# Optimization experiments

Measured on AMD Instinct MI355X. Metric: run time of the kernel, lower is better.

## Reference

```python
import jax, jax.numpy as jnp
import numpy as np

V, BS, E, H, L, FC = 50257, 1024, 768, 12, 6, 4
B, T = 4, 1024
HS = E // H
FF = FC * E
EPS = 1e-5


def setup_inputs() -> dict:
    key = jax.random.key(0)
    ks = jax.random.split(key, 24)
    s = 0.02
    inp = {
        'idx': jax.random.randint(ks[0], (B, T), 0, V),
        'targets': jax.random.randint(ks[1], (B, T), 0, V),
        'tok_emb': jax.random.normal(ks[2], (V, E), jnp.float32) * s,
        'pos_emb': jax.random.normal(ks[3], (BS, E), jnp.float32) * s,
        'Wq': jax.random.normal(ks[4], (L, H, E, HS), jnp.float32) * s,
        'Wk': jax.random.normal(ks[5], (L, H, E, HS), jnp.float32) * s,
        'Wv': jax.random.normal(ks[6], (L, H, E, HS), jnp.float32) * s,
        'Wo': jax.random.normal(ks[7], (L, E, E), jnp.float32) * s,
        'bo': jnp.zeros((L, E), jnp.float32),
        'ln1_s': jnp.ones((L, E), jnp.float32),
        'ln1_b': jnp.zeros((L, E), jnp.float32),
        'ln2_s': jnp.ones((L, E), jnp.float32),
        'ln2_b': jnp.zeros((L, E), jnp.float32),
        'W1': jax.random.normal(ks[8], (L, E, FF), jnp.float32) * s,
        'b1': jnp.zeros((L, FF), jnp.float32),
        'W2': jax.random.normal(ks[9], (L, FF, E), jnp.float32) * s,
        'b2': jnp.zeros((L, E), jnp.float32),
        'lnf_s': jnp.ones((E,), jnp.float32),
        'lnf_b': jnp.zeros((E,), jnp.float32),
        'Wlm': jax.random.normal(ks[10], (E, V), jnp.float32) * s,
        'blm': jnp.zeros((V,), jnp.float32),
    }
    return inp


def _ln(x, scale, bias):
    mu = x.mean(-1, keepdims=True)
    var = ((x - mu) ** 2).mean(-1, keepdims=True)
    return (x - mu) * jax.lax.rsqrt(var + EPS) * scale + bias


def _forward(idx, targets, tok_emb, pos_emb, Wq, Wk, Wv, Wo, bo,
             ln1_s, ln1_b, ln2_s, ln2_b, W1, b1, W2, b2,
             lnf_s, lnf_b, Wlm, blm):
    Bc, Tc = idx.shape
    x = tok_emb[idx] + pos_emb[:Tc]                      # [B,T,E]
    causal = jnp.tril(jnp.ones((Tc, Tc), bool))          # [T,T]

    def block(x, p):
        wq, wk, wv, wo_, bo_, l1s, l1b, l2s, l2b, w1, b1_, w2, b2_ = p
        h = _ln(x, l1s, l1b)
        q = jnp.einsum('bte,hed->bhtd', h, wq)
        k = jnp.einsum('bte,hed->bhtd', h, wk)
        v = jnp.einsum('bte,hed->bhtd', h, wv)
        scores = jnp.einsum('bhtd,bhsd->bhts', q, k) * (HS ** -0.5)
        scores = jnp.where(causal, scores, -jnp.inf)
        att = jax.nn.softmax(scores, axis=-1)            # [B,H,T,T]
        o = jnp.einsum('bhts,bhsd->bhtd', att, v)
        o = o.transpose(0, 2, 1, 3).reshape(Bc, Tc, E)   # concat heads
        x = x + jnp.einsum('bte,ef->btf', o, wo_) + bo_
        h2 = _ln(x, l2s, l2b)
        f = jax.nn.relu(jnp.einsum('bte,ef->btf', h2, w1) + b1_)
        x = x + jnp.einsum('btf,fe->bte', f, w2) + b2_
        return x, None

    layers = (Wq, Wk, Wv, Wo, bo, ln1_s, ln1_b, ln2_s, ln2_b, W1, b1, W2, b2)
    x, _ = jax.lax.scan(block, x, layers)
    x = _ln(x, lnf_s, lnf_b)
    logits = jnp.einsum('bte,ev->btv', x, Wlm) + blm     # [B,T,V]
    logp = jax.nn.log_softmax(logits, axis=-1)
    nll = -jnp.take_along_axis(logp, targets[..., None], axis=-1)[..., 0]
    loss = nll.mean()
    return logits, loss


def reference(idx, targets, tok_emb, pos_emb, Wq, Wk, Wv, Wo, bo,
              ln1_s, ln1_b, ln2_s, ln2_b, W1, b1, W2, b2,
              lnf_s, lnf_b, Wlm, blm):
    return _forward(idx, targets, tok_emb, pos_emb, Wq, Wk, Wv, Wo, bo,
                    ln1_s, ln1_b, ln2_s, ln2_b, W1, b1, W2, b2,
                    lnf_s, lnf_b, Wlm, blm)
```

## Files before the change

kernel.cpp:

```cpp
#include <hip/hip_runtime.h>
#include <hip/hip_bf16.h>
#include <cstdint>
#include <cstddef>

#define NB 4
#define NT 1024
#define NE 768
#define NH 12
#define NHS 64
#define NL 6
#define NFF 3072
#define NV 50257
#define NVP 50304
#define NTOK (NB*NT)
#define NCB_LM (NVP/128)
#define QKVS 2304

typedef __attribute__((ext_vector_type(8))) short short8;
typedef __attribute__((ext_vector_type(4))) float f32x4;
typedef __hip_bfloat16 bf16;

__global__ __launch_bounds__(256) void embed_kernel(
    const int* __restrict__ idx, const float* __restrict__ tok,
    const float* __restrict__ pos, float* __restrict__ x)
{
  int bt = blockIdx.x;
  int token = idx[bt];
  int t = bt & (NT - 1);
  const float* tr = tok + (size_t)token * NE;
  const float* pr = pos + (size_t)t * NE;
  float* xr = x + (size_t)bt * NE;
  for (int i = threadIdx.x; i < NE; i += 256)
    xr[i] = tr[i] + pr[i];
}

__global__ __launch_bounds__(256) void ln_kernel(
    const float* __restrict__ in, const float* __restrict__ sc,
    const float* __restrict__ bi, bf16* __restrict__ out)
{
  int row = blockIdx.x, tid = threadIdx.x;
  const float* xr = in + (size_t)row * NE;
  float v0 = xr[tid], v1 = xr[tid + 256], v2 = xr[tid + 512];
  float s = v0 + v1 + v2;
  float ss = v0 * v0 + v1 * v1 + v2 * v2;
  #pragma unroll
  for (int o = 32; o > 0; o >>= 1) {
    s  += __shfl_xor(s, o);
    ss += __shfl_xor(ss, o);
  }
  __shared__ float r1[4], r2[4];
  if ((tid & 63) == 0) { r1[tid >> 6] = s; r2[tid >> 6] = ss; }
  __syncthreads();
  float tot = r1[0] + r1[1] + r1[2] + r1[3];
  float tss = r2[0] + r2[1] + r2[2] + r2[3];
  float mu  = tot * (1.f / NE);
  float var = tss * (1.f / NE) - mu * mu;
  float rs  = rsqrtf(var + 1e-5f);
  bf16* orow = out + (size_t)row * NE;
  orow[tid]       = __float2bfloat16((v0 - mu) * rs * sc[tid]       + bi[tid]);
  orow[tid + 256] = __float2bfloat16((v1 - mu) * rs * sc[tid + 256] + bi[tid + 256]);
  orow[tid + 512] = __float2bfloat16((v2 - mu) * rs * sc[tid + 512] + bi[tid + 512]);
}

__global__ __launch_bounds__(256) void tconv_kernel(
    const float* __restrict__ src, bf16* __restrict__ dst,
    int R, int Cs, int Cd, int zdiv,
    size_t srcZstr, size_t dstLstr, size_t dstHstr)
{
  __shared__ float t[32][33];
  int z = blockIdx.z;
  int l = z / zdiv, h = z - l * zdiv;
  src += (size_t)z * srcZstr;
  dst += (size_t)l * dstLstr + (size_t)h * dstHstr;
  int c0 = blockIdx.x * 32, r0 = blockIdx.y * 32;
  int tx = threadIdx.x & 31, ty = threadIdx.x >> 5;
  #pragma unroll
  for (int i = 0; i < 32; i += 8) {
    int r = r0 + ty + i, c = c0 + tx;
    t[ty + i][tx] = (c < Cs) ? src[(size_t)r * Cs + c] : 0.f;
  }
  __syncthreads();
  #pragma unroll
  for (int i = 0; i < 32; i += 8) {
    int c = c0 + ty + i, r = r0 + tx;
    if (c < Cd) dst[(size_t)c * R + r] = __float2bfloat16(t[tx][ty + i]);
  }
}

template<int MREP, int DEPTH, bool SWZ>
__global__ __launch_bounds__(256) void pgemm(
    const bf16* __restrict__ A, const bf16* __restrict__ BT,
    float* __restrict__ Cf, bf16* __restrict__ Cbf,
    const float* __restrict__ bias, const float* __restrict__ Rres,
    float* __restrict__ ps,
    int M, int N, int K, int relu, int ncb)
{
  constexpr int BMT = MREP * 32;
  constexpr int AIT = (MREP * 128) / 256;
  constexpr int SWAIT = AIT + 2;
  __shared__ bf16 As[DEPTH][BMT][32];
  __shared__ bf16 Bs[DEPTH][128][32];
  __shared__ float ps2[BMT][2];
  int tid = threadIdx.x;
  int lane = tid & 63;
  int w = __builtin_amdgcn_readfirstlane(tid >> 6);
  int wr = w >> 1, wc = w & 1;
  int row0 = blockIdx.y * BMT;
  int col0 = blockIdx.x * 128;
  int l15 = lane & 15;
  int g8 = (lane >> 4) << 3;
  const int nk = K / 32;

  f32x4 acc[MREP][4] = {};

  auto STAGE = [&](int b, int t) {
    int k0 = t * 32;
    #pragma unroll
    for (int r = 0; r < AIT; ++r) {
      int c = r * 256 + tid;
      int trow = c >> 2;
      int sch = SWZ ? ((c & 3) ^ (trow & 3)) : (c & 3);
      const bf16* ga = A + (size_t)(row0 + trow) * K + k0 + (sch << 3);
      __builtin_amdgcn_global_load_lds(
          (const __attribute__((address_space(1))) void*)ga,
          (__attribute__((address_space(3))) void*)((char*)&As[b][0][0] + (unsigned)c * 16),
          16, 0, 0);
    }
    #pragma unroll
    for (int r = 0; r < 2; ++r) {
      int c = r * 256 + tid;
      int trow = c >> 2;
      int sch = SWZ ? ((c & 3) ^ (trow & 3)) : (c & 3);
      const bf16* gb = BT + (size_t)(col0 + trow) * K + k0 + (sch << 3);
      __builtin_amdgcn_global_load_lds(
          (const __attribute__((address_space(1))) void*)gb,
          (__attribute__((address_space(3))) void*)((char*)&Bs[b][0][0] + (unsigned)c * 16),
          16, 0, 0);
    }
  };

  STAGE(0, 0);
  if (DEPTH == 3 && nk > 1) STAGE(1, 1);

  for (int t = 0; t < nk; ++t) {
    if (DEPTH == 3 && t + 1 < nk) {
      if (SWAIT == 4) asm volatile("s_waitcnt vmcnt(4)" ::: "memory");
      else            asm volatile("s_waitcnt vmcnt(3)" ::: "memory");
    } else {
      asm volatile("s_waitcnt vmcnt(0)" ::: "memory");
    }
    __builtin_amdgcn_s_barrier();
    if (t + DEPTH - 1 < nk) STAGE((t + DEPTH - 1) % DEPTH, t + DEPTH - 1);

    int b = t % DEPTH;
    int sx = SWZ ? ((l15 & 3) << 3) : 0;
    short8 a[MREP], bb[4];
    #pragma unroll
    for (int m = 0; m < MREP; ++m)
      a[m] = *(const short8*)&As[b][wr * (MREP * 16) + m * 16 + l15][g8 ^ sx];
    #pragma unroll
    for (int n = 0; n < 4; ++n)
      bb[n] = *(const short8*)&Bs[b][wc * 64 + n * 16 + l15][g8 ^ sx];
    #pragma unroll
    for (int m = 0; m < MREP; ++m)
      #pragma unroll
      for (int n = 0; n < 4; ++n)
        acc[m][n] = __builtin_amdgcn_mfma_f32_16x16x32_bf16(a[m], bb[n], acc[m][n], 0, 0, 0);
  }

  int cr = lane >> 4;
  int cc = lane & 15;
  #pragma unroll
  for (int m = 0; m < MREP; ++m) {
    #pragma unroll
    for (int n = 0; n < 4; ++n) {
      int col = col0 + wc * 64 + n * 16 + cc;
      if (col >= N) continue;
      float bv = bias ? bias[col] : 0.f;
      #pragma unroll
      for (int e = 0; e < 4; ++e) {
        int row = row0 + wr * (MREP * 16) + m * 16 + cr * 4 + e;
        float v = acc[m][n][e] + bv;
        size_t off = (size_t)row * N + col;
        if (Rres) v += Rres[off];
        if (relu) v = fmaxf(v, 0.f);
        if (Cf)  Cf[off] = v;
        if (Cbf) Cbf[off] = __float2bfloat16(v);
      }
    }
  }

  if (ps) {
    #pragma unroll
    for (int m = 0; m < MREP; ++m) {
      #pragma unroll
      for (int e = 0; e < 4; ++e) {
        float ssum = 0.f;
        #pragma unroll
        for (int n = 0; n < 4; ++n) {
          int col = col0 + wc * 64 + n * 16 + cc;
          float val = (col < N) ? (acc[m][n][e] + (bias ? bias[col] : 0.f)) : -1e30f;
          ssum += __expf(val);
        }
        ssum += __shfl_xor(ssum, 1);
        ssum += __shfl_xor(ssum, 2);
        ssum += __shfl_xor(ssum, 4);
        ssum += __shfl_xor(ssum, 8);
        if (cc == 0) {
          int rl = wr * (MREP * 16) + m * 16 + cr * 4 + e;
          ps2[rl][wc] = ssum;
        }
      }
    }
    __syncthreads();
    for (int i = tid; i < BMT; i += 256) {
      size_t o = (size_t)(row0 + i) * ncb + blockIdx.x;
      ps[o] = ps2[i][0] + ps2[i][1];
    }
  }
}

static __device__ inline unsigned short bfbits(float x) {
  bf16 h = __float2bfloat16(x);
  return *reinterpret_cast<unsigned short*>(&h);
}

__global__ __launch_bounds__(256) void fattn_kernel(
    const bf16* __restrict__ QKV, bf16* __restrict__ O)
{
  __shared__ unsigned short Ks[64][72];
  __shared__ unsigned short Vt[64][72];
  __shared__ unsigned short Pl[4][16][72];
  int qt = blockIdx.x, h = blockIdx.y, b = blockIdx.z;
  int tid = threadIdx.x;
  int lane = tid & 63;
  int w = tid >> 6;
  int l15 = lane & 15, g = lane >> 4;
  int brow = b * NT;
  int qbase = qt * 64;
  int q_loc = w * 16 + l15;

  short8 bq[2];
  {
    const bf16* qp = QKV + (size_t)(brow + qbase + q_loc) * QKVS + h * 64 + g * 8;
    bq[0] = *(const short8*)qp;
    bq[1] = *(const short8*)(qp + 32);
  }

  float m_run = -1e30f, l_run = 0.f;
  f32x4 acc[4] = {};

  for (int kt = 0; kt <= qt; ++kt) {
    int s0 = kt * 64;
    #pragma unroll
    for (int i = 0; i < 2; ++i) {
      int c = tid + i * 256;
      int row = c >> 3, colg = (c & 7) * 8;
      const bf16* kp = QKV + (size_t)(brow + s0 + row) * QKVS + NE + h * 64 + colg;
      const bf16* vp = QKV + (size_t)(brow + s0 + row) * QKVS + 2 * NE + h * 64 + colg;
      short8 kv = *(const short8*)kp;
      short8 vv = *(const short8*)vp;
      *(short8*)&Ks[row][colg] = kv;
      #pragma unroll
      for (int j = 0; j < 8; ++j)
        Vt[colg + j][row] = (unsigned short)vv[j];
    }
    __syncthreads();

    f32x4 sf[4] = {};
    #pragma unroll
    for (int kk = 0; kk < 2; ++kk) {
      #pragma unroll
      for (int m = 0; m < 4; ++m) {
        short8 a = *(const short8*)&Ks[m * 16 + l15][kk * 32 + g * 8];
        sf[m] = __builtin_amdgcn_mfma_f32_16x16x32_bf16(a, bq[kk], sf[m], 0, 0, 0);
      }
    }

    float sv[4][4];
    float mx = -1e30f;
    bool diag = (kt == qt);
    #pragma unroll
    for (int m = 0; m < 4; ++m)
      #pragma unroll
      for (int e = 0; e < 4; ++e) {
        float v = sf[m][e] * 0.125f;
        if (diag) {
          int sl = m * 16 + g * 4 + e;
          if (sl > q_loc) v = -1e30f;
        }
        sv[m][e] = v;
        mx = fmaxf(mx, v);
      }
    mx = fmaxf(mx, __shfl_xor(mx, 16));
    mx = fmaxf(mx, __shfl_xor(mx, 32));
    float m_new = fmaxf(m_run, mx);
    float p[4][4];
    float rs = 0.f;
    #pragma unroll
    for (int m = 0; m < 4; ++m)
      #pragma unroll
      for (int e = 0; e < 4; ++e) {
        float pe = __expf(sv[m][e] - m_new);
        p[m][e] = pe;
        rs += pe;
      }
    rs += __shfl_xor(rs, 16);
    rs += __shfl_xor(rs, 32);
    float sc_old = __expf(m_run - m_new);
    l_run = l_run * sc_old + rs;
    m_run = m_new;
    #pragma unroll
    for (int dm = 0; dm < 4; ++dm)
      #pragma unroll
      for (int e = 0; e < 4; ++e)
        acc[dm][e] *= sc_old;

    #pragma unroll
    for (int m = 0; m < 4; ++m)
      #pragma unroll
      for (int ep = 0; ep < 2; ++ep) {
        unsigned u = (unsigned)bfbits(p[m][2 * ep]) |
                     ((unsigned)bfbits(p[m][2 * ep + 1]) << 16);
        *(unsigned*)&Pl[w][l15][m * 16 + g * 4 + ep * 2] = u;
      }

    #pragma unroll
    for (int ks = 0; ks < 2; ++ks) {
      short8 pb = *(const short8*)&Pl[w][l15][ks * 32 + g * 8];
      #pragma unroll
      for (int dm = 0; dm < 4; ++dm) {
        short8 av = *(const short8*)&Vt[dm * 16 + l15][ks * 32 + g * 8];
        acc[dm] = __builtin_amdgcn_mfma_f32_16x16x32_bf16(av, pb, acc[dm], 0, 0, 0);
      }
    }
    __syncthreads();
  }

  float inv = 1.f / l_run;
  bf16* op = O + (size_t)(brow + qbase + q_loc) * NE + h * 64;
  #pragma unroll
  for (int dm = 0; dm < 4; ++dm)
    #pragma unroll
    for (int ep = 0; ep < 2; ++ep) {
      int d = dm * 16 + g * 4 + ep * 2;
      unsigned u = (unsigned)bfbits(acc[dm][2 * ep] * inv) |
                   ((unsigned)bfbits(acc[dm][2 * ep + 1] * inv) << 16);
      *(unsigned*)((unsigned short*)op + d) = u;
    }
}

__global__ __launch_bounds__(128) void nll_finish(
    const float* __restrict__ ps,
    const float* __restrict__ logits, const int* __restrict__ targets,
    float* __restrict__ nll)
{
  int row = blockIdx.x, tid = threadIdx.x;
  float s = 0.f;
  for (int i = tid; i < NCB_LM; i += 128)
    s += ps[(size_t)row * NCB_LM + i];
  #pragma unroll
  for (int o = 32; o > 0; o >>= 1) s += __shfl_xor(s, o);
  __shared__ float ss[2];
  if ((tid & 63) == 0) ss[tid >> 6] = s;
  __syncthreads();
  if (tid == 0) {
    float S = ss[0] + ss[1];
    float tgt = logits[(size_t)row * NV + targets[row]];
    nll[row] = logf(S) - tgt;
  }
}

__global__ __launch_bounds__(256) void loss_kernel(
    const float* __restrict__ nll, float* __restrict__ out)
{
  int tid = threadIdx.x;
  float s = 0.f;
  for (int i = tid; i < NTOK; i += 256) s += nll[i];
  #pragma unroll
  for (int o = 32; o > 0; o >>= 1) s += __shfl_xor(s, o);
  __shared__ float red[4];
  if ((tid & 63) == 0) red[tid >> 6] = s;
  __syncthreads();
  if (tid == 0) out[0] = (red[0] + red[1] + red[2] + red[3]) * (1.f / NTOK);
}

static inline void gemm(const bf16* A, const bf16* BT,
                        float* Cf, bf16* Cbf,
                        const float* bias, const float* Rres, float* ps,
                        int M, int N, int Npad, int K, int relu,
                        int mrep, hipStream_t st)
{
  int ncb = Npad / 128;
  dim3 g(ncb, M / (mrep * 32));
  if (mrep == 4)
    pgemm<4, 2, true><<<g, dim3(256), 0, st>>>(A, BT, Cf, Cbf, bias, Rres, ps, M, N, K, relu, ncb);
  else
    pgemm<2, 2, true><<<g, dim3(256), 0, st>>>(A, BT, Cf, Cbf, bias, Rres, ps, M, N, K, relu, ncb);
}

extern "C" void kernel_launch(void* const* d_in, const int* in_sizes, int n_in,
                              void* d_out, int out_size, void* d_ws, size_t ws_size,
                              hipStream_t stream)
{
  const int*   idx     = (const int*)  d_in[0];
  const int*   targets = (const int*)  d_in[1];
  const float* tok_emb = (const float*)d_in[2];
  const float* pos_emb = (const float*)d_in[3];
  const float* Wq      = (const float*)d_in[4];
  const float* Wk      = (const float*)d_in[5];
  const float* Wv      = (const float*)d_in[6];
  const float* Wo      = (const float*)d_in[7];
  const float* bo      = (const float*)d_in[8];
  const float* ln1_s   = (const float*)d_in[9];
  const float* ln1_b   = (const float*)d_in[10];
  const float* ln2_s   = (const float*)d_in[11];
  const float* ln2_b   = (const float*)d_in[12];
  const float* W1      = (const float*)d_in[13];
  const float* b1      = (const float*)d_in[14];
  const float* W2      = (const float*)d_in[15];
  const float* b2      = (const float*)d_in[16];
  const float* lnf_s   = (const float*)d_in[17];
  const float* lnf_b   = (const float*)d_in[18];
  const float* Wlm     = (const float*)d_in[19];
  const float* blm     = (const float*)d_in[20];
  float* out = (float*)d_out;

  const size_t XE = (size_t)NTOK * NE;
  char* p = (char*)d_ws;
  float* x     = (float*)p;         p += XE * 4;
  bf16* h_bf   = (bf16*)p;          p += XE * 2;
  bf16* qkv_bf = (bf16*)p;          p += (size_t)NTOK * QKVS * 2;
  bf16* att_bf = (bf16*)p;          p += XE * 2;
  bf16* f_bf   = (bf16*)p;          p += (size_t)NTOK * NFF * 2;
  bf16* wqkv_a = (bf16*)p;          p += (size_t)NL * QKVS * NE * 2;
  bf16* wto_a  = (bf16*)p;          p += (size_t)NL * NE * NE * 2;
  bf16* wt1_a  = (bf16*)p;          p += (size_t)NL * NFF * NE * 2;
  bf16* wt2_a  = (bf16*)p;          p += (size_t)NL * NE * NFF * 2;
  bf16* wtlm   = (bf16*)p;          p += (size_t)NVP * NE * 2;
  float* psb   = (float*)p;         p += (size_t)NTOK * NCB_LM * 4;
  float* nll   = (float*)p;         p += (size_t)NTOK * 4;

  embed_kernel<<<dim3(NTOK), dim3(256), 0, stream>>>(idx, tok_emb, pos_emb, x);

  tconv_kernel<<<dim3(2, 24, NL * NH), dim3(256), 0, stream>>>(
      Wq, wqkv_a, NE, NHS, NHS, NH,
      (size_t)NE * NHS, (size_t)QKVS * NE, (size_t)NHS * NE);
  tconv_kernel<<<dim3(2, 24, NL * NH), dim3(256), 0, stream>>>(
      Wk, wqkv_a + (size_t)NE * NE, NE, NHS, NHS, NH,
      (size_t)NE * NHS, (size_t)QKVS * NE, (size_t)NHS * NE);
  tconv_kernel<<<dim3(2, 24, NL * NH), dim3(256), 0, stream>>>(
      Wv, wqkv_a + (size_t)2 * NE * NE, NE, NHS, NHS, NH,
      (size_t)NE * NHS, (size_t)QKVS * NE, (size_t)NHS * NE);
  tconv_kernel<<<dim3(24, 24, NL), dim3(256), 0, stream>>>(
      Wo, wto_a, NE, NE, NE, 1, (size_t)NE * NE, (size_t)NE * NE, 0);
  tconv_kernel<<<dim3(96, 24, NL), dim3(256), 0, stream>>>(
      W1, wt1_a, NE, NFF, NFF, 1, (size_t)NE * NFF, (size_t)NFF * NE, 0);
  tconv_kernel<<<dim3(24, 96, NL), dim3(256), 0, stream>>>(
      W2, wt2_a, NFF, NE, NE, 1, (size_t)NFF * NE, (size_t)NE * NFF, 0);
  tconv_kernel<<<dim3(NVP / 32, 24, 1), dim3(256), 0, stream>>>(
      Wlm, wtlm, NE, NV, NVP, 1, 0, 0, 0);

  for (int l = 0; l < NL; ++l) {
    ln_kernel<<<dim3(NTOK), dim3(256), 0, stream>>>(x, ln1_s + l*NE, ln1_b + l*NE, h_bf);

    gemm(h_bf, wqkv_a + (size_t)l * QKVS * NE, nullptr, qkv_bf, nullptr, nullptr, nullptr,
         NTOK, QKVS, QKVS, NE, 0, 4, stream);

    fattn_kernel<<<dim3(NT / 64, NH, NB), dim3(256), 0, stream>>>(qkv_bf, att_bf);

    gemm(att_bf, wto_a + (size_t)l * NE * NE, x, nullptr, bo + l*NE, x, nullptr,
         NTOK, NE, NE, NE, 0, 2, stream);

    ln_kernel<<<dim3(NTOK), dim3(256), 0, stream>>>(x, ln2_s + l*NE, ln2_b + l*NE, h_bf);

    gemm(h_bf, wt1_a + (size_t)l * NFF * NE, nullptr, f_bf, b1 + l*NFF, nullptr, nullptr,
         NTOK, NFF, NFF, NE, 1, 4, stream);
    gemm(f_bf, wt2_a + (size_t)l * NE * NFF, x, nullptr, b2 + l*NE, x, nullptr,
         NTOK, NE, NE, NFF, 0, 2, stream);
  }

  ln_kernel<<<dim3(NTOK), dim3(256), 0, stream>>>(x, lnf_s, lnf_b, h_bf);

  {
    dim3 g(NCB_LM, NTOK / 128);
    pgemm<4, 3, false><<<g, dim3(256), 0, stream>>>(
        h_bf, wtlm, out, nullptr, blm, nullptr, psb,
        NTOK, NV, NE, 0, NCB_LM);
  }

  nll_finish<<<dim3(NTOK), dim3(128), 0, stream>>>(psb, out, targets, nll);
  loss_kernel<<<dim3(1), dim3(256), 0, stream>>>(nll, out + (size_t)NTOK * NV);
}
```

Baseline: 2.344 ms.

## Store residual in bf16, restructure GEMM pipeline, widen attention tiles with lazy rescale

The residual stream x moves from fp32 to bf16 storage in embed, layernorm and the residual-add epilogues, halving the traffic for those reads and writes. The GEMM drops to a double-buffered loop that issues the next stage before computing on the current one and reuses the A buffer for the softmax partial sums. Attention now uses 128-query blocks with 512 threads, prefetches the next K/V tile into registers, and rescales the accumulator only when the running max rises by more than 8. The LM-head weight transpose is moved after the transformer layers. A bf16 residual loses precision across layers, and the lazy rescale relies on the later normalisation by l_run to stay correct.

```diff
diff --git a/kernel.cpp b/kernel.cpp
--- a/kernel.cpp
+++ b/kernel.cpp
@@ -22,25 +22,27 @@
 
 __global__ __launch_bounds__(256) void embed_kernel(
     const int* __restrict__ idx, const float* __restrict__ tok,
-    const float* __restrict__ pos, float* __restrict__ x)
+    const float* __restrict__ pos, bf16* __restrict__ x)
 {
   int bt = blockIdx.x;
   int token = idx[bt];
   int t = bt & (NT - 1);
   const float* tr = tok + (size_t)token * NE;
   const float* pr = pos + (size_t)t * NE;
-  float* xr = x + (size_t)bt * NE;
+  bf16* xr = x + (size_t)bt * NE;
   for (int i = threadIdx.x; i < NE; i += 256)
-    xr[i] = tr[i] + pr[i];
+    xr[i] = __float2bfloat16(tr[i] + pr[i]);
 }
 
 __global__ __launch_bounds__(256) void ln_kernel(
-    const float* __restrict__ in, const float* __restrict__ sc,
+    const bf16* __restrict__ in, const float* __restrict__ sc,
     const float* __restrict__ bi, bf16* __restrict__ out)
 {
   int row = blockIdx.x, tid = threadIdx.x;
-  const float* xr = in + (size_t)row * NE;
-  float v0 = xr[tid], v1 = xr[tid + 256], v2 = xr[tid + 512];
+  const bf16* xr = in + (size_t)row * NE;
+  float v0 = __bfloat162float(xr[tid]);
+  float v1 = __bfloat162float(xr[tid + 256]);
+  float v2 = __bfloat162float(xr[tid + 512]);
   float s = v0 + v1 + v2;
   float ss = v0 * v0 + v1 * v1 + v2 * v2;
   #pragma unroll
@@ -87,20 +89,19 @@
   }
 }
 
-template<int MREP, int DEPTH, bool SWZ>
-__global__ __launch_bounds__(256) void pgemm(
+template<int MREP, bool SWZ>
+__global__ __launch_bounds__(256) void plgemm(
     const bf16* __restrict__ A, const bf16* __restrict__ BT,
     float* __restrict__ Cf, bf16* __restrict__ Cbf,
-    const float* __restrict__ bias, const float* __restrict__ Rres,
+    const float* __restrict__ bias, const bf16* __restrict__ Rres,
     float* __restrict__ ps,
     int M, int N, int K, int relu, int ncb)
 {
   constexpr int BMT = MREP * 32;
-  constexpr int AIT = (MREP * 128) / 256;
-  constexpr int SWAIT = AIT + 2;
-  __shared__ bf16 As[DEPTH][BMT][32];
-  __shared__ bf16 Bs[DEPTH][128][32];
-  __shared__ float ps2[BMT][2];
+  constexpr int AIT = MREP / 2;
+  __shared__ bf16 As[2][BMT][32];
+  __shared__ bf16 Bs[2][128][32];
+  float (*ps2)[2] = reinterpret_cast<float(*)[2]>(&As[0][0][0]);
   int tid = threadIdx.x;
   int lane = tid & 63;
   int w = __builtin_amdgcn_readfirstlane(tid >> 6);
@@ -108,13 +109,13 @@
   int row0 = blockIdx.y * BMT;
   int col0 = blockIdx.x * 128;
   int l15 = lane & 15;
-  int g8 = (lane >> 4) << 3;
+  int g = lane >> 4;
+  int rcol = ((g ^ (SWZ ? (l15 & 3) : 0)) << 3);
+
+  f32x4 acc[MREP][4] = {};
   const int nk = K / 32;
 
-  f32x4 acc[MREP][4] = {};
-
-  auto STAGE = [&](int b, int t) {
-    int k0 = t * 32;
+  auto STAGE = [&](int b, int k0) {
     #pragma unroll
     for (int r = 0; r < AIT; ++r) {
       int c = r * 256 + tid;
@@ -140,27 +141,36 @@
   };
 
   STAGE(0, 0);
-  if (DEPTH == 3 && nk > 1) STAGE(1, 1);
-
-  for (int t = 0; t < nk; ++t) {
-    if (DEPTH == 3 && t + 1 < nk) {
-      if (SWAIT == 4) asm volatile("s_waitcnt vmcnt(4)" ::: "memory");
-      else            asm volatile("s_waitcnt vmcnt(3)" ::: "memory");
-    } else {
-      asm volatile("s_waitcnt vmcnt(0)" ::: "memory");
-    }
+  asm volatile("s_waitcnt vmcnt(0)" ::: "memory");
+  __builtin_amdgcn_s_barrier();
+
+  int cur = 0;
+  for (int t = 0; t < nk - 1; ++t) {
+    STAGE(cur ^ 1, (t + 1) * 32);
+    short8 a[MREP], bb[4];
+    #pragma unroll
+    for (int m = 0; m < MREP; ++m)
+      a[m] = *(const short8*)&As[cur][wr * (MREP * 16) + m * 16 + l15][rcol];
+    #pragma unroll
+    for (int n = 0; n < 4; ++n)
+      bb[n] = *(const short8*)&Bs[cur][wc * 64 + n * 16 + l15][rcol];
+    #pragma unroll
+    for (int m = 0; m < MREP; ++m)
+      #pragma unroll
+      for (int n = 0; n < 4; ++n)
+        acc[m][n] = __builtin_amdgcn_mfma_f32_16x16x32_bf16(a[m], bb[n], acc[m][n], 0, 0, 0);
+    asm volatile("s_waitcnt vmcnt(0)" ::: "memory");
     __builtin_amdgcn_s_barrier();
-    if (t + DEPTH - 1 < nk) STAGE((t + DEPTH - 1) % DEPTH, t + DEPTH - 1);
-
-    int b = t % DEPTH;
-    int sx = SWZ ? ((l15 & 3) << 3) : 0;
+    cur ^= 1;
+  }
+  {
     short8 a[MREP], bb[4];
     #pragma unroll
     for (int m = 0; m < MREP; ++m)
-      a[m] = *(const short8*)&As[b][wr * (MREP * 16) + m * 16 + l15][g8 ^ sx];
+      a[m] = *(const short8*)&As[cur][wr * (MREP * 16) + m * 16 + l15][rcol];
     #pragma unroll
     for (int n = 0; n < 4; ++n)
-      bb[n] = *(const short8*)&Bs[b][wc * 64 + n * 16 + l15][g8 ^ sx];
+      bb[n] = *(const short8*)&Bs[cur][wc * 64 + n * 16 + l15][rcol];
     #pragma unroll
     for (int m = 0; m < MREP; ++m)
       #pragma unroll
@@ -182,7 +192,7 @@
         int row = row0 + wr * (MREP * 16) + m * 16 + cr * 4 + e;
         float v = acc[m][n][e] + bv;
         size_t off = (size_t)row * N + col;
-        if (Rres) v += Rres[off];
+        if (Rres) v += __bfloat162float(Rres[off]);
         if (relu) v = fmaxf(v, 0.f);
         if (Cf)  Cf[off] = v;
         if (Cbf) Cbf[off] = __float2bfloat16(v);
@@ -206,10 +216,7 @@
         ssum += __shfl_xor(ssum, 2);
         ssum += __shfl_xor(ssum, 4);
         ssum += __shfl_xor(ssum, 8);
-        if (cc == 0) {
-          int rl = wr * (MREP * 16) + m * 16 + cr * 4 + e;
-          ps2[rl][wc] = ssum;
-        }
+        if (cc == 0) ps2[wr * (MREP * 16) + m * 16 + cr * 4 + e][wc] = ssum;
       }
     }
     __syncthreads();
@@ -225,19 +232,19 @@
   return *reinterpret_cast<unsigned short*>(&h);
 }
 
-__global__ __launch_bounds__(256) void fattn_kernel(
+__global__ __launch_bounds__(512) void fattn_kernel(
     const bf16* __restrict__ QKV, bf16* __restrict__ O)
 {
   __shared__ unsigned short Ks[64][72];
   __shared__ unsigned short Vt[64][72];
-  __shared__ unsigned short Pl[4][16][72];
+  __shared__ unsigned short Pl[8][16][72];
   int qt = blockIdx.x, h = blockIdx.y, b = blockIdx.z;
   int tid = threadIdx.x;
   int lane = tid & 63;
   int w = tid >> 6;
   int l15 = lane & 15, g = lane >> 4;
   int brow = b * NT;
-  int qbase = qt * 64;
+  int qbase = qt * 128;
   int q_loc = w * 16 + l15;
 
   short8 bq[2];
@@ -247,25 +254,28 @@
     bq[1] = *(const short8*)(qp + 32);
   }
 
+  short8 kreg, vreg;
+  int rowt = tid >> 3, colgt = (tid & 7) * 8;
+
+  auto LOADKV = [&](int kt) {
+    int s0 = kt * 64;
+    const bf16* base = QKV + (size_t)(brow + s0 + rowt) * QKVS + h * 64;
+    kreg = *(const short8*)(base + NE + colgt);
+    vreg = *(const short8*)(base + 2 * NE + colgt);
+  };
+
   float m_run = -1e30f, l_run = 0.f;
   f32x4 acc[4] = {};
-
-  for (int kt = 0; kt <= qt; ++kt) {
-    int s0 = kt * 64;
-    #pragma unroll
-    for (int i = 0; i < 2; ++i) {
-      int c = tid + i * 256;
-      int row = c >> 3, colg = (c & 7) * 8;
-      const bf16* kp = QKV + (size_t)(brow + s0 + row) * QKVS + NE + h * 64 + colg;
-      const bf16* vp = QKV + (size_t)(brow + s0 + row) * QKVS + 2 * NE + h * 64 + colg;
-      short8 kv = *(const short8*)kp;
-      short8 vv = *(const short8*)vp;
-      *(short8*)&Ks[row][colg] = kv;
-      #pragma unroll
-      for (int j = 0; j < 8; ++j)
-        Vt[colg + j][row] = (unsigned short)vv[j];
-    }
+  const int nkt = 2 * qt + 2;
+
+  LOADKV(0);
+  for (int kt = 0; kt < nkt; ++kt) {
+    *(short8*)&Ks[rowt][colgt] = kreg;
+    #pragma unroll
+    for (int j = 0; j < 8; ++j)
+      Vt[colgt + j][rowt] = (unsigned short)vreg[j];
     __syncthreads();
+    if (kt + 1 < nkt) LOADKV(kt + 1);
 
     f32x4 sf[4] = {};
     #pragma unroll
@@ -279,14 +289,15 @@
 
     float sv[4][4];
     float mx = -1e30f;
-    bool diag = (kt == qt);
+    bool diag = (kt >= 2 * qt);
+    int sbase = kt * 64 - qbase;
     #pragma unroll
     for (int m = 0; m < 4; ++m)
       #pragma unroll
       for (int e = 0; e < 4; ++e) {
         float v = sf[m][e] * 0.125f;
         if (diag) {
-          int sl = m * 16 + g * 4 + e;
+          int sl = sbase + m * 16 + g * 4 + e;
           if (sl > q_loc) v = -1e30f;
         }
         sv[m][e] = v;
@@ -294,27 +305,32 @@
       }
     mx = fmaxf(mx, __shfl_xor(mx, 16));
     mx = fmaxf(mx, __shfl_xor(mx, 32));
-    float m_new = fmaxf(m_run, mx);
+
+    if (!__all(mx - m_run <= 8.f)) {
+      float m_new = fmaxf(m_run, mx);
+      float sc_old = __expf(m_run - m_new);
+      l_run *= sc_old;
+      #pragma unroll
+      for (int dm = 0; dm < 4; ++dm)
+        #pragma unroll
+        for (int e = 0; e < 4; ++e)
+          acc[dm][e] *= sc_old;
+      m_run = m_new;
+    }
+
     float p[4][4];
     float rs = 0.f;
     #pragma unroll
     for (int m = 0; m < 4; ++m)
       #pragma unroll
       for (int e = 0; e < 4; ++e) {
-        float pe = __expf(sv[m][e] - m_new);
+        float pe = __expf(sv[m][e] - m_run);
         p[m][e] = pe;
         rs += pe;
       }
     rs += __shfl_xor(rs, 16);
     rs += __shfl_xor(rs, 32);
-    float sc_old = __expf(m_run - m_new);
-    l_run = l_run * sc_old + rs;
-    m_run = m_new;
-    #pragma unroll
-    for (int dm = 0; dm < 4; ++dm)
-      #pragma unroll
-      for (int e = 0; e < 4; ++e)
-        acc[dm][e] *= sc_old;
+    l_run += rs;
 
     #pragma unroll
     for (int m = 0; m < 4; ++m)
@@ -387,16 +403,18 @@
 
 static inline void gemm(const bf16* A, const bf16* BT,
                         float* Cf, bf16* Cbf,
-                        const float* bias, const float* Rres, float* ps,
+                        const float* bias, const bf16* Rres, float* ps,
                         int M, int N, int Npad, int K, int relu,
                         int mrep, hipStream_t st)
 {
   int ncb = Npad / 128;
-  dim3 g(ncb, M / (mrep * 32));
-  if (mrep == 4)
-    pgemm<4, 2, true><<<g, dim3(256), 0, st>>>(A, BT, Cf, Cbf, bias, Rres, ps, M, N, K, relu, ncb);
-  else
-    pgemm<2, 2, true><<<g, dim3(256), 0, st>>>(A, BT, Cf, Cbf, bias, Rres, ps, M, N, K, relu, ncb);
+  if (mrep == 4) {
+    dim3 g(ncb, M / 128);
+    plgemm<4, true><<<g, dim3(256), 0, st>>>(A, BT, Cf, Cbf, bias, Rres, ps, M, N, K, relu, ncb);
+  } else {
+    dim3 g(ncb, M / 64);
+    plgemm<2, true><<<g, dim3(256), 0, st>>>(A, BT, Cf, Cbf, bias, Rres, ps, M, N, K, relu, ncb);
+  }
 }
 
 extern "C" void kernel_launch(void* const* d_in, const int* in_sizes, int n_in,
@@ -428,7 +446,7 @@
 
   const size_t XE = (size_t)NTOK * NE;
   char* p = (char*)d_ws;
-  float* x     = (float*)p;         p += XE * 4;
+  bf16* x_bf   = (bf16*)p;          p += XE * 2;
   bf16* h_bf   = (bf16*)p;          p += XE * 2;
   bf16* qkv_bf = (bf16*)p;          p += (size_t)NTOK * QKVS * 2;
   bf16* att_bf = (bf16*)p;          p += XE * 2;
@@ -441,7 +459,7 @@
   float* psb   = (float*)p;         p += (size_t)NTOK * NCB_LM * 4;
   float* nll   = (float*)p;         p += (size_t)NTOK * 4;
 
-  embed_kernel<<<dim3(NTOK), dim3(256), 0, stream>>>(idx, tok_emb, pos_emb, x);
+  embed_kernel<<<dim3(NTOK), dim3(256), 0, stream>>>(idx, tok_emb, pos_emb, x_bf);
 
   tconv_kernel<<<dim3(2, 24, NL * NH), dim3(256), 0, stream>>>(
       Wq, wqkv_a, NE, NHS, NHS, NH,
@@ -458,33 +476,34 @@
       W1, wt1_a, NE, NFF, NFF, 1, (size_t)NE * NFF, (size_t)NFF * NE, 0);
   tconv_kernel<<<dim3(24, 96, NL), dim3(256), 0, stream>>>(
       W2, wt2_a, NFF, NE, NE, 1, (size_t)NFF * NE, (size_t)NE * NFF, 0);
+
+  for (int l = 0; l < NL; ++l) {
+    ln_kernel<<<dim3(NTOK), dim3(256), 0, stream>>>(x_bf, ln1_s + l*NE, ln1_b + l*NE, h_bf);
+
+    gemm(h_bf, wqkv_a + (size_t)l * QKVS * NE, nullptr, qkv_bf, nullptr, nullptr, nullptr,
+         NTOK, QKVS, QKVS, NE, 0, 4, stream);
+
+    fattn_kernel<<<dim3(NT / 128, NH, NB), dim3(512), 0, stream>>>(qkv_bf, att_bf);
+
+    gemm(att_bf, wto_a + (size_t)l * NE * NE, nullptr, x_bf, bo + l*NE, x_bf, nullptr,
+         NTOK, NE, NE, NE, 0, 2, stream);
+
+    ln_kernel<<<dim3(NTOK), dim3(256), 0, stream>>>(x_bf, ln2_s + l*NE, ln2_b + l*NE, h_bf);
+
+    gemm(h_bf, wt1_a + (size_t)l * NFF * NE, nullptr, f_bf, b1 + l*NFF, nullptr, nullptr,
+         NTOK, NFF, NFF, NE, 1, 4, stream);
+    gemm(f_bf, wt2_a + (size_t)l * NE * NFF, nullptr, x_bf, b2 + l*NE, x_bf, nullptr,
+         NTOK, NE, NE, NFF, 0, 2, stream);
+  }
+
+  ln_kernel<<<dim3(NTOK), dim3(256), 0, stream>>>(x_bf, lnf_s, lnf_b, h_bf);
+
   tconv_kernel<<<dim3(NVP / 32, 24, 1), dim3(256), 0, stream>>>(
       Wlm, wtlm, NE, NV, NVP, 1, 0, 0, 0);
 
-  for (int l = 0; l < NL; ++l) {
-    ln_kernel<<<dim3(NTOK), dim3(256), 0, stream>>>(x, ln1_s + l*NE, ln1_b + l*NE, h_bf);
-
-    gemm(h_bf, wqkv_a + (size_t)l * QKVS * NE, nullptr, qkv_bf, nullptr, nullptr, nullptr,
-         NTOK, QKVS, QKVS, NE, 0, 4, stream);
-
-    fattn_kernel<<<dim3(NT / 64, NH, NB), dim3(256), 0, stream>>>(qkv_bf, att_bf);
-
-    gemm(att_bf, wto_a + (size_t)l * NE * NE, x, nullptr, bo + l*NE, x, nullptr,
-         NTOK, NE, NE, NE, 0, 2, stream);
-
-    ln_kernel<<<dim3(NTOK), dim3(256), 0, stream>>>(x, ln2_s + l*NE, ln2_b + l*NE, h_bf);
-
-    gemm(h_bf, wt1_a + (size_t)l * NFF * NE, nullptr, f_bf, b1 + l*NFF, nullptr, nullptr,
-         NTOK, NFF, NFF, NE, 1, 4, stream);
-    gemm(f_bf, wt2_a + (size_t)l * NE * NFF, x, nullptr, b2 + l*NE, x, nullptr,
-         NTOK, NE, NE, NFF, 0, 2, stream);
-  }
-
-  ln_kernel<<<dim3(NTOK), dim3(256), 0, stream>>>(x, lnf_s, lnf_b, h_bf);
-
   {
     dim3 g(NCB_LM, NTOK / 128);
-    pgemm<4, 3, false><<<g, dim3(256), 0, stream>>>(
+    plgemm<4, false><<<g, dim3(256), 0, stream>>>(
         h_bf, wtlm, out, nullptr, blm, nullptr, psb,
         NTOK, NV, NE, 0, NCB_LM);
   }
```

Measured after the change: 2.202 ms. -6.0%, faster.
